# Kernel optimization log

Measured on AMD Instinct MI355X. Metric: run time of the kernel, lower is better.

## Reference

```python
import jax, jax.numpy as jnp
import numpy as np

B, C, H, W = 32, 64, 64, 64
K = 512  # n_embeddings
D = 64   # embedding_dim


def setup_inputs() -> dict:
    key = jax.random.key(0)
    k1, k2 = jax.random.split(key)
    inputs = jax.random.normal(k1, (B, C, H, W), dtype=jnp.float32)
    embedding = jax.random.normal(k2, (K, D), dtype=jnp.float32)
    weight = jnp.ones((K,), dtype=jnp.float32)
    return {"inputs": inputs, "embedding": embedding, "weight": weight}


def reference(inputs, embedding, weight):
    # NCHW -> NHWC, flatten to [N, D]
    x = jnp.transpose(inputs, (0, 2, 3, 1))  # [B,H,W,D]
    input_shape = x.shape
    flat = x.reshape(-1, D)                  # [N,D], N = B*H*W
    n = flat.shape[0]

    usage = jnp.sum(weight >= 0.01)

    # squared Euclidean distances (argmin-equivalent to torch.cdist)
    d2 = (jnp.sum(flat * flat, axis=1, keepdims=True)
          - 2.0 * (flat @ embedding.T)
          + jnp.sum(embedding * embedding, axis=1))  # [N,K]
    indices = jnp.argmin(d2, axis=1)                 # [N]

    # one-hot assignment stats (scatter -> bincount form)
    counts = jnp.zeros((K,), dtype=flat.dtype).at[indices].add(1.0)
    avg_probs = counts / n
    perplexity = jnp.exp(-jnp.sum(avg_probs * jnp.log(avg_probs + 1e-10)))

    # straight-through quantization
    q = embedding[indices].reshape(input_shape)      # [B,H,W,D]
    quantized = jax.lax.stop_gradient(q) + x - jax.lax.stop_gradient(x)

    commitment_loss = jnp.mean((jax.lax.stop_gradient(quantized) - x) ** 2)

    quantized_nchw = jnp.transpose(quantized, (0, 3, 1, 2))
    return quantized_nchw, commitment_loss, perplexity, usage, indices
```

## Files before the change

kernel.cpp:

```cpp
#include <hip/hip_runtime.h>


typedef __attribute__((ext_vector_type(8))) _Float16 f16x8;
typedef __attribute__((ext_vector_type(4))) float f32x4;
typedef unsigned int uint;
typedef unsigned short ushort;

namespace {
constexpr int kC = 64, kH = 64, kW = 64;
constexpr int kK = 512, kD = 64;
constexpr int kHW = kH * kW;
constexpr int kCHW = kC * kHW;
constexpr int kN = 32 * kHW;
constexpr int kQElems = 32 * kC * kHW;
constexpr uint kGapFP = 21u;
}

__device__ __forceinline__ ushort hb(_Float16 h) { return __builtin_bit_cast(ushort, h); }
__device__ __forceinline__ uint umin(uint a, uint b) { return a < b ? a : b; }
__device__ __forceinline__ uint umax(uint a, uint b) { return a > b ? a : b; }

__global__ __launch_bounds__(512) void vq_prep(const float* __restrict__ emb,
                                               ushort* __restrict__ embh,
                                               ushort* __restrict__ embl,
                                               float* __restrict__ enorm,
                                               uint* __restrict__ counts,
                                               uint* __restrict__ flag_count) {
  const int k = threadIdx.x;
  const float4* __restrict__ ep4 = (const float4*)(emb + k * kD);
  float s = 0.f;
#pragma unroll
  for (int j = 0; j < kD / 4; ++j) {
    const float4 v = ep4[j];
    s = fmaf(v.x, v.x, s); s = fmaf(v.y, v.y, s);
    s = fmaf(v.z, v.z, s); s = fmaf(v.w, v.w, s);
    const float e0 = v.x * 2048.f, e1 = v.y * 2048.f;
    const float e2 = v.z * 2048.f, e3 = v.w * 2048.f;
    const _Float16 h0 = (_Float16)e0, h1 = (_Float16)e1;
    const _Float16 h2 = (_Float16)e2, h3 = (_Float16)e3;
    const _Float16 l0 = (_Float16)(e0 - (float)h0);
    const _Float16 l1 = (_Float16)(e1 - (float)h1);
    const _Float16 l2 = (_Float16)(e2 - (float)h2);
    const _Float16 l3 = (_Float16)(e3 - (float)h3);
    *(uint2*)(embh + k * kD + 4 * j) =
        uint2{(uint)hb(h0) | ((uint)hb(h1) << 16), (uint)hb(h2) | ((uint)hb(h3) << 16)};
    *(uint2*)(embl + k * kD + 4 * j) =
        uint2{(uint)hb(l0) | ((uint)hb(l1) << 16), (uint)hb(l2) | ((uint)hb(l3) << 16)};
  }
  enorm[k] = s;
  counts[k] = 0u;
  if (k == 0) *flag_count = 0u;
}

__global__ __launch_bounds__(512, 4) void vq_assign(
    const float* __restrict__ in, const ushort* __restrict__ embh,
    const ushort* __restrict__ embl, const float* __restrict__ enorm,
    float* __restrict__ idx_out, uint* __restrict__ counts,
    float* __restrict__ partial, uint* __restrict__ flag_count,
    uint* __restrict__ flags, uint flag_cap) {
  __shared__ __align__(16) ushort ebh[128 * 64];
  __shared__ __align__(16) ushort ebl[128 * 64];
  __shared__ __align__(16) ushort xbh[128 * 64];
  __shared__ __align__(16) ushort xbl[128 * 64];
  __shared__ uint mm1[4][128], mm2[4][128];
  __shared__ float xnp[4][128];
  __shared__ uint hist[512];

  const int tid = threadIdx.x;
  const int lane = tid & 63;
  const int wv = __builtin_amdgcn_readfirstlane(tid >> 6);
  const int ph = wv >> 2;
  const int cs = wv & 3;
  const int c = lane & 15;
  const int g = lane >> 4;

  const int blk = blockIdx.x;
  const int bb = blk >> 5;
  const int hw0 = (blk & 31) << 7;
  const float* __restrict__ xp = in + (size_t)bb * kCHW + hw0 + ph * 64;

  hist[tid] = 0u;

  float en_pre[8];
#pragma unroll
  for (int q = 0; q < 4; ++q)
#pragma unroll
    for (int ct = 0; ct < 2; ++ct)
      en_pre[q * 2 + ct] = (enorm[q * 128 + cs * 32 + ct * 16 + c] + 256.f) * 2048.f;

  {
    const int p = lane;
    uint uh[8], ul[8];
    float xn = 0.f;
#pragma unroll
    for (int j = 0; j < 8; ++j) {
      const float f0 = xp[(size_t)(cs * 16 + 2 * j) * kHW + p];
      const float f1 = xp[(size_t)(cs * 16 + 2 * j + 1) * kHW + p];
      xn = fmaf(f0, f0, xn);
      xn = fmaf(f1, f1, xn);
      const float m0 = -2.f * f0, m1f = -2.f * f1;
      const _Float16 h0 = (_Float16)m0, h1 = (_Float16)m1f;
      const _Float16 l0 = (_Float16)(m0 - (float)h0);
      const _Float16 l1 = (_Float16)(m1f - (float)h1);
      uh[j] = (uint)hb(h0) | ((uint)hb(h1) << 16);
      ul[j] = (uint)hb(l0) | ((uint)hb(l1) << 16);
    }
    const int row = ph * 64 + p;
    const int swz = (row & 7) << 4;
    const int o0 = (row * 128 + cs * 32) ^ swz;
    const int o1 = (row * 128 + cs * 32 + 16) ^ swz;
    *(uint4*)((char*)xbh + o0) = uint4{uh[0], uh[1], uh[2], uh[3]};
    *(uint4*)((char*)xbh + o1) = uint4{uh[4], uh[5], uh[6], uh[7]};
    *(uint4*)((char*)xbl + o0) = uint4{ul[0], ul[1], ul[2], ul[3]};
    *(uint4*)((char*)xbl + o1) = uint4{ul[4], ul[5], ul[6], ul[7]};
    xnp[cs][row] = xn;
  }

  auto stageE = [&](int q) {
#pragma unroll
    for (int i = 0; i < 2; ++i) {
      const int chunk = tid + i * 512;
      const int row = chunk >> 3, cc = chunk & 7;
      const int dsto = (row * 128 + cc * 16) ^ ((row & 7) << 4);
      *(uint4*)((char*)ebh + dsto) = *(const uint4*)(embh + q * 128 * 64 + chunk * 8);
      *(uint4*)((char*)ebl + dsto) = *(const uint4*)(embl + q * 128 * 64 + chunk * 8);
    }
  };
  stageE(0);
  __syncthreads();

  uint m1[16], m2[16];
#pragma unroll
  for (int i = 0; i < 16; ++i) { m1[i] = 0xFFFFFFFFu; m2[i] = 0xFFFFFFFFu; }

#pragma unroll
  for (int q = 0; q < 4; ++q) {
    if (q) {
      __syncthreads();
      stageE(q);
      __syncthreads();
    }
    f16x8 bh[2][2], bl[2][2];
#pragma unroll
    for (int ct = 0; ct < 2; ++ct)
#pragma unroll
      for (int s = 0; s < 2; ++s) {
        const int rowb = cs * 32 + ct * 16 + c;
        const int off = (rowb * 128 + g * 16 + s * 64) ^ ((rowb & 7) << 4);
        bh[ct][s] = *(const f16x8*)((const char*)ebh + off);
        bl[ct][s] = *(const f16x8*)((const char*)ebl + off);
      }
#pragma unroll
    for (int rt = 0; rt < 4; ++rt) {
      f16x8 ah[2], al[2];
#pragma unroll
      for (int s = 0; s < 2; ++s) {
        const int row = ph * 64 + rt * 16 + c;
        const int off = (row * 128 + g * 16 + s * 64) ^ ((row & 7) << 4);
        ah[s] = *(const f16x8*)((const char*)xbh + off);
        al[s] = *(const f16x8*)((const char*)xbl + off);
      }
#pragma unroll
      for (int ct = 0; ct < 2; ++ct) {
        const float en = en_pre[q * 2 + ct];
        f32x4 acc = {en, en, en, en};
        acc = __builtin_amdgcn_mfma_f32_16x16x32_f16(ah[0], bh[ct][0], acc, 0, 0, 0);
        acc = __builtin_amdgcn_mfma_f32_16x16x32_f16(ah[1], bh[ct][1], acc, 0, 0, 0);
        acc = __builtin_amdgcn_mfma_f32_16x16x32_f16(ah[0], bl[ct][0], acc, 0, 0, 0);
        acc = __builtin_amdgcn_mfma_f32_16x16x32_f16(ah[1], bl[ct][1], acc, 0, 0, 0);
        acc = __builtin_amdgcn_mfma_f32_16x16x32_f16(al[0], bh[ct][0], acc, 0, 0, 0);
        acc = __builtin_amdgcn_mfma_f32_16x16x32_f16(al[1], bh[ct][1], acc, 0, 0, 0);
        const uint kor = (uint)(q * 128 + cs * 32 + ct * 16 + c);
#pragma unroll
        for (int r = 0; r < 4; ++r) {
          const uint u = ((uint)acc[r] << 9) | kor;
          const int i = rt * 4 + r;
          const uint t = umax(m1[i], u);
          m1[i] = umin(m1[i], u);
          m2[i] = umin(m2[i], t);
        }
      }
    }
  }

#pragma unroll
  for (int i = 0; i < 16; ++i) {
    uint a1 = m1[i], a2 = m2[i];
#pragma unroll
    for (int off = 1; off < 16; off <<= 1) {
      const uint o1 = __shfl_xor(a1, off, 64);
      const uint o2 = __shfl_xor(a2, off, 64);
      const uint t = umax(a1, o1);
      a1 = umin(a1, o1);
      a2 = umin(umin(a2, o2), t);
    }
    m1[i] = a1; m2[i] = a2;
  }

  if (c == 0) {
#pragma unroll
    for (int i = 0; i < 16; ++i) {
      const int p = ph * 64 + (i >> 2) * 16 + g * 4 + (i & 3);
      mm1[cs][p] = m1[i];
      mm2[cs][p] = m2[i];
    }
  }
  __syncthreads();

  if (tid < 128) {
    uint a1 = mm1[0][tid], a2 = mm2[0][tid];
#pragma unroll
    for (int s = 1; s < 4; ++s) {
      const uint u1 = mm1[s][tid], u2 = mm2[s][tid];
      const uint t = umax(a1, u1);
      a1 = umin(a1, u1);
      a2 = umin(umin(a2, u2), t);
    }
    const uint bidx = a1 & 511u;
    idx_out[blk * 128 + tid] = (float)bidx;
    if (((a2 >> 9) - (a1 >> 9)) < kGapFP) {
      const uint slot = atomicAdd(flag_count, 1u);
      if (slot < flag_cap) flags[slot] = (uint)(blk * 128 + tid);
    }
    atomicAdd(&hist[bidx], 1u);

    const float xnorm = (xnp[0][tid] + xnp[1][tid]) + (xnp[2][tid] + xnp[3][tid]);
    float d2 = fmaf((float)(a1 >> 9), 1.f / 2048.f, -256.f) + xnorm;
#pragma unroll
    for (int off = 32; off > 0; off >>= 1) d2 += __shfl_down(d2, off, 64);
    if ((tid & 63) == 0) partial[blk * 2 + (tid >> 6)] = d2;
  }
  __syncthreads();
  if (hist[tid]) atomicAdd(&counts[tid], hist[tid]);
}

__global__ __launch_bounds__(256) void vq_refine(const float* __restrict__ in,
                                                 const float* __restrict__ emb,
                                                 const uint* __restrict__ flag_count,
                                                 const uint* __restrict__ flags,
                                                 uint flag_cap,
                                                 float* __restrict__ idx_out) {
  uint cnt = *flag_count;
  if (cnt > flag_cap) cnt = flag_cap;
  const int lane = threadIdx.x & 63;
  const uint wave_id = blockIdx.x * 4u + (threadIdx.x >> 6);
  const uint wave_stride = gridDim.x * 4u;

  for (uint i = wave_id; i < cnt; i += wave_stride) {
    const int n = (int)flags[i];
    const int b = n >> 12;
    const int hw = n & 4095;
    const float* __restrict__ xp = in + (size_t)b * kCHW + hw;

    float xr[kD];
#pragma unroll
    for (int d = 0; d < kD; ++d) xr[d] = xp[(size_t)d * kHW];

    double best = 1e300;
    int bidx = 0;
#pragma unroll 1
    for (int kk = 0; kk < 8; ++kk) {
      const int k = lane * 8 + kk;
      const float4* __restrict__ ep4 = (const float4*)(emb + k * kD);
      double s0 = 0.0, s1 = 0.0;
#pragma unroll
      for (int j = 0; j < kD / 4; ++j) {
        const float4 e = ep4[j];
        const double d0 = (double)xr[4 * j + 0] - (double)e.x;
        const double d1 = (double)xr[4 * j + 1] - (double)e.y;
        const double d2 = (double)xr[4 * j + 2] - (double)e.z;
        const double d3 = (double)xr[4 * j + 3] - (double)e.w;
        s0 = fma(d0, d0, s0);
        s1 = fma(d1, d1, s1);
        s0 = fma(d2, d2, s0);
        s1 = fma(d3, d3, s1);
      }
      const double s = s0 + s1;
      if (s < best) { best = s; bidx = k; }
    }
#pragma unroll
    for (int off = 32; off > 0; off >>= 1) {
      const double ob = __shfl_xor(best, off, 64);
      const int oi = __shfl_xor(bidx, off, 64);
      if (ob < best || (ob == best && oi < bidx)) { best = ob; bidx = oi; }
    }
    if (lane == 0) idx_out[n] = (float)bidx;
  }
}

__global__ __launch_bounds__(512) void vq_finalize(const float* __restrict__ weight,
                                                   const uint* __restrict__ counts,
                                                   const float* __restrict__ partial,
                                                   float* __restrict__ out_scalars) {
  __shared__ float red[512];
  const int t = threadIdx.x;

  const float avg = (float)counts[t] / (float)kN;
  red[t] = avg * logf(avg + 1e-10f);
  __syncthreads();
#pragma unroll
  for (int off = 256; off > 0; off >>= 1) {
    if (t < off) red[t] += red[t + off];
    __syncthreads();
  }
  const float perp = expf(-red[0]);
  __syncthreads();

  red[t] = (partial[t] + partial[t + 512]) + (partial[t + 1024] + partial[t + 1536]);
  __syncthreads();
#pragma unroll
  for (int off = 256; off > 0; off >>= 1) {
    if (t < off) red[t] += red[t + off];
    __syncthreads();
  }
  const float loss = red[0] / (float)((long long)kN * (long long)kD);
  __syncthreads();

  red[t] = (weight[t] >= 0.01f) ? 1.f : 0.f;
  __syncthreads();
#pragma unroll
  for (int off = 256; off > 0; off >>= 1) {
    if (t < off) red[t] += red[t + off];
    __syncthreads();
  }
  if (t == 0) {
    out_scalars[0] = loss;
    out_scalars[1] = perp;
    out_scalars[2] = red[0];
  }
}

__global__ __launch_bounds__(256) void vq_gather(const float* __restrict__ emb,
                                                 const float* __restrict__ idx_f,
                                                 float* __restrict__ outq) {
  const int q4 = blockIdx.x * 256 + threadIdx.x;
  const int base = q4 * 4;
  const int w0 = base & 63;
  const int h = (base >> 6) & 63;
  const int c = (base >> 12) & 63;
  const int b = base >> 18;
  const int n0 = (b << 12) | (h << 6) | w0;
  const float4 iv = *(const float4*)(idx_f + n0);
  float4 o;
  o.x = emb[(int)iv.x * kD + c];
  o.y = emb[(int)iv.y * kD + c];
  o.z = emb[(int)iv.z * kD + c];
  o.w = emb[(int)iv.w * kD + c];
  *(float4*)(outq + base) = o;
}

extern "C" void kernel_launch(void* const* d_in, const int* in_sizes, int n_in,
                              void* d_out, int out_size, void* d_ws, size_t ws_size,
                              hipStream_t stream) {
  const float* in = (const float*)d_in[0];
  const float* emb = (const float*)d_in[1];
  const float* weight = (const float*)d_in[2];
  float* out = (float*)d_out;

  float* ws_f = (float*)d_ws;
  uint* ws_u = (uint*)d_ws;
  ushort* embh = (ushort*)d_ws;
  ushort* embl = embh + kK * kD;
  float* enorm = ws_f + 32768;
  uint* counts = ws_u + 33280;
  float* partial = ws_f + 33792;
  uint* flag_count = ws_u + 35840;
  uint* flags = ws_u + 35841;
  const size_t ws_elems = ws_size / 4;
  const uint flag_cap =
      (ws_elems > 35841)
          ? (uint)((ws_elems - 35841 < (size_t)kN) ? ws_elems - 35841 : (size_t)kN)
          : 0u;

  float* outq = out;
  float* out_scalars = out + kQElems;
  float* idx_out = out + kQElems + 3;

  vq_prep<<<1, 512, 0, stream>>>(emb, embh, embl, enorm, counts, flag_count);
  vq_assign<<<kN / 128, 512, 0, stream>>>(in, embh, embl, enorm, idx_out, counts,
                                          partial, flag_count, flags, flag_cap);
  vq_refine<<<256, 256, 0, stream>>>(in, emb, flag_count, flags, flag_cap, idx_out);
  vq_gather<<<kQElems / 1024, 256, 0, stream>>>(emb, idx_out, outq);
  vq_finalize<<<1, 512, 0, stream>>>(weight, counts, partial, out_scalars);
}
```

Baseline: 104.9 us.

## Fuse quantized gather into assign kernel and double-buffer codebook via global_load_lds

Removes the separate gather kernel: the assign kernel now writes the quantized NCHW output directly from a transposed codebook copy, using indices kept in shared memory. The refine kernel rewrites output rows for any indices it corrects. The codebook is pre-swizzled in the prep kernel and streamed into LDS in 64-row stages, double-buffered with async global_load_lds, so the extra sync-and-copy phases of the old staging go away. This costs a larger workspace, a transposed codebook written from a single block, and more LDS per block, which may affect occupancy.

Result: faster. 94.95 us (-9.5%).

```diff
diff --git a/kernel.cpp b/kernel.cpp
--- a/kernel.cpp
+++ b/kernel.cpp
@@ -20,51 +20,71 @@
 __device__ __forceinline__ uint umin(uint a, uint b) { return a < b ? a : b; }
 __device__ __forceinline__ uint umax(uint a, uint b) { return a > b ? a : b; }
 
+__device__ __forceinline__ void gld16(const void* g, void* l) {
+  __builtin_amdgcn_global_load_lds(
+      (const __attribute__((address_space(1))) uint*)g,
+      (__attribute__((address_space(3))) uint*)l, 16, 0, 0);
+}
+
 __global__ __launch_bounds__(512) void vq_prep(const float* __restrict__ emb,
-                                               ushort* __restrict__ embh,
-                                               ushort* __restrict__ embl,
+                                               ushort* __restrict__ embPh,
+                                               ushort* __restrict__ embPl,
+                                               float* __restrict__ embT,
                                                float* __restrict__ enorm,
                                                uint* __restrict__ counts,
                                                uint* __restrict__ flag_count) {
   const int k = threadIdx.x;
   const float4* __restrict__ ep4 = (const float4*)(emb + k * kD);
+  float ev[kD];
+  uint uh[32], ul[32];
   float s = 0.f;
 #pragma unroll
   for (int j = 0; j < kD / 4; ++j) {
     const float4 v = ep4[j];
+    ev[4 * j] = v.x; ev[4 * j + 1] = v.y; ev[4 * j + 2] = v.z; ev[4 * j + 3] = v.w;
     s = fmaf(v.x, v.x, s); s = fmaf(v.y, v.y, s);
     s = fmaf(v.z, v.z, s); s = fmaf(v.w, v.w, s);
-    const float e0 = v.x * 2048.f, e1 = v.y * 2048.f;
-    const float e2 = v.z * 2048.f, e3 = v.w * 2048.f;
-    const _Float16 h0 = (_Float16)e0, h1 = (_Float16)e1;
-    const _Float16 h2 = (_Float16)e2, h3 = (_Float16)e3;
-    const _Float16 l0 = (_Float16)(e0 - (float)h0);
-    const _Float16 l1 = (_Float16)(e1 - (float)h1);
-    const _Float16 l2 = (_Float16)(e2 - (float)h2);
-    const _Float16 l3 = (_Float16)(e3 - (float)h3);
-    *(uint2*)(embh + k * kD + 4 * j) =
-        uint2{(uint)hb(h0) | ((uint)hb(h1) << 16), (uint)hb(h2) | ((uint)hb(h3) << 16)};
-    *(uint2*)(embl + k * kD + 4 * j) =
-        uint2{(uint)hb(l0) | ((uint)hb(l1) << 16), (uint)hb(l2) | ((uint)hb(l3) << 16)};
-  }
+#pragma unroll
+    for (int t = 0; t < 2; ++t) {
+      const float e0 = ev[4 * j + 2 * t] * 2048.f;
+      const float e1 = ev[4 * j + 2 * t + 1] * 2048.f;
+      const _Float16 h0 = (_Float16)e0, h1 = (_Float16)e1;
+      const _Float16 l0 = (_Float16)(e0 - (float)h0);
+      const _Float16 l1 = (_Float16)(e1 - (float)h1);
+      uh[2 * j + t] = (uint)hb(h0) | ((uint)hb(h1) << 16);
+      ul[2 * j + t] = (uint)hb(l0) | ((uint)hb(l1) << 16);
+    }
+  }
+  uint4* __restrict__ ph4 = (uint4*)embPh;
+  uint4* __restrict__ pl4 = (uint4*)embPl;
+#pragma unroll
+  for (int cc = 0; cc < 8; ++cc) {
+    const int dst = k * 8 + (cc ^ (k & 7));
+    ph4[dst] = uint4{uh[4 * cc], uh[4 * cc + 1], uh[4 * cc + 2], uh[4 * cc + 3]};
+    pl4[dst] = uint4{ul[4 * cc], ul[4 * cc + 1], ul[4 * cc + 2], ul[4 * cc + 3]};
+  }
+#pragma unroll
+  for (int c = 0; c < kD; ++c) embT[c * kK + k] = ev[c];
   enorm[k] = s;
   counts[k] = 0u;
   if (k == 0) *flag_count = 0u;
 }
 
 __global__ __launch_bounds__(512, 4) void vq_assign(
-    const float* __restrict__ in, const ushort* __restrict__ embh,
-    const ushort* __restrict__ embl, const float* __restrict__ enorm,
-    float* __restrict__ idx_out, uint* __restrict__ counts,
+    const float* __restrict__ in, const ushort* __restrict__ embPh,
+    const ushort* __restrict__ embPl, const float* __restrict__ embT,
+    const float* __restrict__ enorm, float* __restrict__ idx_out,
+    float* __restrict__ outq, uint* __restrict__ counts,
     float* __restrict__ partial, uint* __restrict__ flag_count,
     uint* __restrict__ flags, uint flag_cap) {
-  __shared__ __align__(16) ushort ebh[128 * 64];
-  __shared__ __align__(16) ushort ebl[128 * 64];
   __shared__ __align__(16) ushort xbh[128 * 64];
   __shared__ __align__(16) ushort xbl[128 * 64];
+  __shared__ __align__(16) ushort ebh[2][4096];
+  __shared__ __align__(16) ushort ebl[2][4096];
   __shared__ uint mm1[4][128], mm2[4][128];
   __shared__ float xnp[4][128];
   __shared__ uint hist[512];
+  __shared__ uint fidx[128];
 
   const int tid = threadIdx.x;
   const int lane = tid & 63;
@@ -81,12 +101,18 @@
 
   hist[tid] = 0u;
 
+  auto stageE = [&](int buf, int st) {
+    const char* gh = (const char*)embPh + st * 8192 + wv * 1024 + lane * 16;
+    const char* gl = (const char*)embPl + st * 8192 + wv * 1024 + lane * 16;
+    gld16(gh, (char*)&ebh[buf][0] + wv * 1024);
+    gld16(gl, (char*)&ebl[buf][0] + wv * 1024);
+  };
+  stageE(0, 0);
+
   float en_pre[8];
 #pragma unroll
-  for (int q = 0; q < 4; ++q)
-#pragma unroll
-    for (int ct = 0; ct < 2; ++ct)
-      en_pre[q * 2 + ct] = (enorm[q * 128 + cs * 32 + ct * 16 + c] + 256.f) * 2048.f;
+  for (int st = 0; st < 8; ++st)
+    en_pre[st] = (enorm[st * 64 + cs * 16 + c] + 256.f) * 2048.f;
 
   {
     const int p = lane;
@@ -116,40 +142,26 @@
     xnp[cs][row] = xn;
   }
 
-  auto stageE = [&](int q) {
-#pragma unroll
-    for (int i = 0; i < 2; ++i) {
-      const int chunk = tid + i * 512;
-      const int row = chunk >> 3, cc = chunk & 7;
-      const int dsto = (row * 128 + cc * 16) ^ ((row & 7) << 4);
-      *(uint4*)((char*)ebh + dsto) = *(const uint4*)(embh + q * 128 * 64 + chunk * 8);
-      *(uint4*)((char*)ebl + dsto) = *(const uint4*)(embl + q * 128 * 64 + chunk * 8);
-    }
-  };
-  stageE(0);
-  __syncthreads();
-
   uint m1[16], m2[16];
 #pragma unroll
   for (int i = 0; i < 16; ++i) { m1[i] = 0xFFFFFFFFu; m2[i] = 0xFFFFFFFFu; }
 
 #pragma unroll
-  for (int q = 0; q < 4; ++q) {
-    if (q) {
-      __syncthreads();
-      stageE(q);
-      __syncthreads();
-    }
-    f16x8 bh[2][2], bl[2][2];
-#pragma unroll
-    for (int ct = 0; ct < 2; ++ct)
-#pragma unroll
-      for (int s = 0; s < 2; ++s) {
-        const int rowb = cs * 32 + ct * 16 + c;
-        const int off = (rowb * 128 + g * 16 + s * 64) ^ ((rowb & 7) << 4);
-        bh[ct][s] = *(const f16x8*)((const char*)ebh + off);
-        bl[ct][s] = *(const f16x8*)((const char*)ebl + off);
-      }
+  for (int st = 0; st < 8; ++st) {
+    __syncthreads();
+    if (st < 7) stageE((st & 1) ^ 1, st + 1);
+
+    const int rowb = cs * 16 + c;
+    const int swb = (rowb & 7) << 4;
+    const int ob0 = (rowb * 128 + g * 16) ^ swb;
+    const int ob1 = (rowb * 128 + g * 16 + 64) ^ swb;
+    const int bsel = st & 1;
+    const f16x8 bh0 = *(const f16x8*)((const char*)&ebh[bsel][0] + ob0);
+    const f16x8 bh1 = *(const f16x8*)((const char*)&ebh[bsel][0] + ob1);
+    const f16x8 bl0 = *(const f16x8*)((const char*)&ebl[bsel][0] + ob0);
+    const f16x8 bl1 = *(const f16x8*)((const char*)&ebl[bsel][0] + ob1);
+    const float en = en_pre[st];
+    const uint kor = (uint)(st * 64 + cs * 16 + c);
 #pragma unroll
     for (int rt = 0; rt < 4; ++rt) {
       f16x8 ah[2], al[2];
@@ -160,25 +172,20 @@
         ah[s] = *(const f16x8*)((const char*)xbh + off);
         al[s] = *(const f16x8*)((const char*)xbl + off);
       }
-#pragma unroll
-      for (int ct = 0; ct < 2; ++ct) {
-        const float en = en_pre[q * 2 + ct];
-        f32x4 acc = {en, en, en, en};
-        acc = __builtin_amdgcn_mfma_f32_16x16x32_f16(ah[0], bh[ct][0], acc, 0, 0, 0);
-        acc = __builtin_amdgcn_mfma_f32_16x16x32_f16(ah[1], bh[ct][1], acc, 0, 0, 0);
-        acc = __builtin_amdgcn_mfma_f32_16x16x32_f16(ah[0], bl[ct][0], acc, 0, 0, 0);
-        acc = __builtin_amdgcn_mfma_f32_16x16x32_f16(ah[1], bl[ct][1], acc, 0, 0, 0);
-        acc = __builtin_amdgcn_mfma_f32_16x16x32_f16(al[0], bh[ct][0], acc, 0, 0, 0);
-        acc = __builtin_amdgcn_mfma_f32_16x16x32_f16(al[1], bh[ct][1], acc, 0, 0, 0);
-        const uint kor = (uint)(q * 128 + cs * 32 + ct * 16 + c);
-#pragma unroll
-        for (int r = 0; r < 4; ++r) {
-          const uint u = ((uint)acc[r] << 9) | kor;
-          const int i = rt * 4 + r;
-          const uint t = umax(m1[i], u);
-          m1[i] = umin(m1[i], u);
-          m2[i] = umin(m2[i], t);
-        }
+      f32x4 acc = {en, en, en, en};
+      acc = __builtin_amdgcn_mfma_f32_16x16x32_f16(ah[0], bh0, acc, 0, 0, 0);
+      acc = __builtin_amdgcn_mfma_f32_16x16x32_f16(ah[1], bh1, acc, 0, 0, 0);
+      acc = __builtin_amdgcn_mfma_f32_16x16x32_f16(ah[0], bl0, acc, 0, 0, 0);
+      acc = __builtin_amdgcn_mfma_f32_16x16x32_f16(ah[1], bl1, acc, 0, 0, 0);
+      acc = __builtin_amdgcn_mfma_f32_16x16x32_f16(al[0], bh0, acc, 0, 0, 0);
+      acc = __builtin_amdgcn_mfma_f32_16x16x32_f16(al[1], bh1, acc, 0, 0, 0);
+#pragma unroll
+      for (int r = 0; r < 4; ++r) {
+        const uint u = ((uint)acc[r] << 9) | kor;
+        const int i = rt * 4 + r;
+        const uint t = umax(m1[i], u);
+        m1[i] = umin(m1[i], u);
+        m2[i] = umin(m2[i], t);
       }
     }
   }
@@ -217,6 +224,7 @@
       a2 = umin(umin(a2, u2), t);
     }
     const uint bidx = a1 & 511u;
+    fidx[tid] = bidx;
     idx_out[blk * 128 + tid] = (float)bidx;
     if (((a2 >> 9) - (a1 >> 9)) < kGapFP) {
       const uint slot = atomicAdd(flag_count, 1u);
@@ -232,6 +240,23 @@
   }
   __syncthreads();
   if (hist[tid]) atomicAdd(&counts[tid], hist[tid]);
+
+  {
+    const int ch = tid >> 3;
+    const int wq = tid & 7;
+    const float* __restrict__ tr = embT + ch * kK;
+    float* __restrict__ oq = outq + (size_t)bb * kCHW + (size_t)ch * kHW + hw0 + wq * 16;
+#pragma unroll
+    for (int i = 0; i < 4; ++i) {
+      const int p0 = wq * 16 + i * 4;
+      float4 v;
+      v.x = tr[fidx[p0 + 0]];
+      v.y = tr[fidx[p0 + 1]];
+      v.z = tr[fidx[p0 + 2]];
+      v.w = tr[fidx[p0 + 3]];
+      *(float4*)(oq + i * 4) = v;
+    }
+  }
 }
 
 __global__ __launch_bounds__(256) void vq_refine(const float* __restrict__ in,
@@ -239,7 +264,8 @@
                                                  const uint* __restrict__ flag_count,
                                                  const uint* __restrict__ flags,
                                                  uint flag_cap,
-                                                 float* __restrict__ idx_out) {
+                                                 float* __restrict__ idx_out,
+                                                 float* __restrict__ outq) {
   uint cnt = *flag_count;
   if (cnt > flag_cap) cnt = flag_cap;
   const int lane = threadIdx.x & 63;
@@ -285,6 +311,7 @@
       if (ob < best || (ob == best && oi < bidx)) { best = ob; bidx = oi; }
     }
     if (lane == 0) idx_out[n] = (float)bidx;
+    outq[(size_t)b * kCHW + (size_t)lane * kHW + hw] = emb[bidx * kD + lane];
   }
 }
 
@@ -328,25 +355,6 @@
     out_scalars[1] = perp;
     out_scalars[2] = red[0];
   }
-}
-
-__global__ __launch_bounds__(256) void vq_gather(const float* __restrict__ emb,
-                                                 const float* __restrict__ idx_f,
-                                                 float* __restrict__ outq) {
-  const int q4 = blockIdx.x * 256 + threadIdx.x;
-  const int base = q4 * 4;
-  const int w0 = base & 63;
-  const int h = (base >> 6) & 63;
-  const int c = (base >> 12) & 63;
-  const int b = base >> 18;
-  const int n0 = (b << 12) | (h << 6) | w0;
-  const float4 iv = *(const float4*)(idx_f + n0);
-  float4 o;
-  o.x = emb[(int)iv.x * kD + c];
-  o.y = emb[(int)iv.y * kD + c];
-  o.z = emb[(int)iv.z * kD + c];
-  o.w = emb[(int)iv.w * kD + c];
-  *(float4*)(outq + base) = o;
 }
 
 extern "C" void kernel_launch(void* const* d_in, const int* in_sizes, int n_in,
@@ -359,27 +367,29 @@
 
   float* ws_f = (float*)d_ws;
   uint* ws_u = (uint*)d_ws;
-  ushort* embh = (ushort*)d_ws;
-  ushort* embl = embh + kK * kD;
-  float* enorm = ws_f + 32768;
-  uint* counts = ws_u + 33280;
-  float* partial = ws_f + 33792;
-  uint* flag_count = ws_u + 35840;
-  uint* flags = ws_u + 35841;
+  ushort* embPh = (ushort*)d_ws;
+  ushort* embPl = embPh + kK * kD;
+  float* embT = ws_f + 32768;
+  float* enorm = ws_f + 65536;
+  uint* counts = ws_u + 66048;
+  float* partial = ws_f + 66560;
+  uint* flag_count = ws_u + 68608;
+  uint* flags = ws_u + 68609;
   const size_t ws_elems = ws_size / 4;
   const uint flag_cap =
-      (ws_elems > 35841)
-          ? (uint)((ws_elems - 35841 < (size_t)kN) ? ws_elems - 35841 : (size_t)kN)
+      (ws_elems > 68609)
+          ? (uint)((ws_elems - 68609 < (size_t)kN) ? ws_elems - 68609 : (size_t)kN)
           : 0u;
 
   float* outq = out;
   float* out_scalars = out + kQElems;
   float* idx_out = out + kQElems + 3;
 
-  vq_prep<<<1, 512, 0, stream>>>(emb, embh, embl, enorm, counts, flag_count);
-  vq_assign<<<kN / 128, 512, 0, stream>>>(in, embh, embl, enorm, idx_out, counts,
-                                          partial, flag_count, flags, flag_cap);
-  vq_refine<<<256, 256, 0, stream>>>(in, emb, flag_count, flags, flag_cap, idx_out);
-  vq_gather<<<kQElems / 1024, 256, 0, stream>>>(emb, idx_out, outq);
+  vq_prep<<<1, 512, 0, stream>>>(emb, embPh, embPl, embT, enorm, counts, flag_count);
+  vq_assign<<<kN / 128, 512, 0, stream>>>(in, embPh, embPl, embT, enorm, idx_out,
+                                          outq, counts, partial, flag_count, flags,
+                                          flag_cap);
+  vq_refine<<<256, 256, 0, stream>>>(in, emb, flag_count, flags, flag_cap,
+                                     idx_out, outq);
   vq_finalize<<<1, 512, 0, stream>>>(weight, counts, partial, out_scalars);
 }
```
